# Kernel tuning notes

Measured on AMD Instinct MI355X. Metric: run time of the kernel, lower is better.

Reference implementation:

```python
import jax, jax.numpy as jnp
import numpy as np

B, S, D, H = 2, 2048, 1024, 16
DH = D // H  # head dim = 64


def setup_inputs() -> dict:
    key = jax.random.key(0)
    ks = jax.random.split(key, 8)
    q = jax.random.normal(ks[0], (B, S, D), dtype=jnp.float32)
    k = jax.random.normal(ks[1], (B, S, D), dtype=jnp.float32)
    v = jax.random.normal(ks[2], (B, S, D), dtype=jnp.float32)
    attn_mask = jax.random.randint(ks[3], (1, 1, S, S), 0, 2, dtype=jnp.int32)
    sc = 1.0 / np.sqrt(D)
    Wq = (jax.random.normal(ks[4], (D, D), dtype=jnp.float32) * sc)
    Wk = (jax.random.normal(ks[5], (D, D), dtype=jnp.float32) * sc)
    Wv = (jax.random.normal(ks[6], (D, D), dtype=jnp.float32) * sc)
    Wo = (jax.random.normal(ks[7], (D, D), dtype=jnp.float32) * sc)
    return {"q": q, "k": k, "v": v, "attn_mask": attn_mask,
            "Wq": Wq, "Wk": Wk, "Wv": Wv, "Wo": Wo}


def reference(q, k, v, attn_mask, Wq, Wk, Wv, Wo):
    bs = q.shape[0]
    # torch Linear: y = x @ W.T ; split heads -> [B, H, S, DH]
    qh = (q @ Wq.T).reshape(bs, -1, H, DH).transpose(0, 2, 1, 3)
    kh = (k @ Wk.T).reshape(bs, -1, H, DH).transpose(0, 2, 1, 3)
    vh = (v @ Wv.T).reshape(bs, -1, H, DH).transpose(0, 2, 1, 3)
    # scaled dot-product attention with explicit [B,H,S,S] scores
    scores = jnp.einsum('bhqd,bhkd->bhqk', qh, kh) / jnp.sqrt(
        jnp.asarray(DH, dtype=qh.dtype))
    scores = jnp.where(attn_mask == 0, jnp.asarray(-1e34, scores.dtype), scores)
    attn = jax.nn.softmax(scores, axis=-1)
    out = jnp.einsum('bhqk,bhkd->bhqd', attn, vh)
    out = out.transpose(0, 2, 1, 3).reshape(bs, -1, H * DH)
    out = out @ Wo.T
    return (out, attn)
```

## Files before the change

### kernel.cpp

```cpp
#include <hip/hip_runtime.h>
#include <stdint.h>

#define S_ 2048
#define NKT_ 32
#define LP 72

typedef short bf16x8 __attribute__((ext_vector_type(8)));
typedef float f32x4 __attribute__((ext_vector_type(4)));

__device__ __forceinline__ short f2bf(float x) {
  union { float f; uint32_t u; } v; v.f = x;
  uint32_t r = v.u + 0x7fffu + ((v.u >> 16) & 1u);
  return (short)(r >> 16);
}
__device__ __forceinline__ float bf2f(short s) {
  union { uint32_t u; float f; } v; v.u = ((uint32_t)(uint16_t)s) << 16;
  return v.f;
}

__device__ __forceinline__ void gload16(const void* g, void* l) {
  __builtin_amdgcn_global_load_lds((const __attribute__((address_space(1))) void*)g,
                                   (__attribute__((address_space(3))) void*)l, 16, 0, 0);
}

__global__ __launch_bounds__(256) void detect_dtype(const uint32_t* __restrict__ q,
                                                    uint32_t* __restrict__ flag) {
  __shared__ int cnt;
  int t = threadIdx.x;
  if (t == 0) cnt = 0;
  __syncthreads();
  uint32_t w = q[t];
  int e = (int)((w >> 7) & 0xFF);
  int hit = (e >= 100 && e <= 141) ? 1 : 0;
  atomicAdd(&cnt, hit);
  __syncthreads();
  if (t == 0) *flag = (cnt >= 200) ? 0u : 1u;
}

__device__ __forceinline__ void cvt_body(const void* __restrict__ src,
                                         short* __restrict__ d, long n8, int f) {
  long i = (long)blockIdx.x * 256 + threadIdx.x;
  const long stride = (long)gridDim.x * 256;
  if (f) {
    const f32x4* s = (const f32x4*)src;
    for (; i < n8; i += stride) {
      f32x4 a = s[2 * i], b = s[2 * i + 1];
      bf16x8 r;
      r[0] = f2bf(a[0]); r[1] = f2bf(a[1]); r[2] = f2bf(a[2]); r[3] = f2bf(a[3]);
      r[4] = f2bf(b[0]); r[5] = f2bf(b[1]); r[6] = f2bf(b[2]); r[7] = f2bf(b[3]);
      *(bf16x8*)(d + i * 8) = r;
    }
  } else {
    const bf16x8* s = (const bf16x8*)src;
    for (; i < n8; i += stride) *(bf16x8*)(d + i * 8) = s[i];
  }
}

__global__ __launch_bounds__(256) void to_bf16_batch(
    const void* __restrict__ q, const void* __restrict__ k, const void* __restrict__ v,
    const void* __restrict__ wq, const void* __restrict__ wk, const void* __restrict__ wv,
    short* __restrict__ dst, const uint32_t* __restrict__ flag) {
  const void* src; long n8; long doff;
  switch (blockIdx.y) {
    case 0:  src = q;  n8 = 524288; doff = 0;        break;
    case 1:  src = k;  n8 = 524288; doff = 4194304;  break;
    case 2:  src = v;  n8 = 524288; doff = 8388608;  break;
    case 3:  src = wq; n8 = 131072; doff = 12582912; break;
    case 4:  src = wk; n8 = 131072; doff = 13631488; break;
    default: src = wv; n8 = 131072; doff = 14680064; break;
  }
  cvt_body(src, dst + doff, n8, (int)*flag);
}

__global__ __launch_bounds__(256) void to_bf16_one(const void* __restrict__ src,
                                                   short* __restrict__ dst, long n8,
                                                   const uint32_t* __restrict__ flag) {
  cvt_body(src, dst, n8, (int)*flag);
}

template <int MODE>
__device__ __forceinline__ void gemm_body(short* sA, short* sW,
    const short* __restrict__ A, const short* __restrict__ W,
    short* __restrict__ dst, float* __restrict__ dstF, int outf) {
  const int tid = threadIdx.x;
  const int wave = tid >> 6, lane = tid & 63;
  const int quad = lane >> 4, l16 = lane & 15;
  const int m0 = blockIdx.x * 128, n0 = blockIdx.y * 128;
  const int wm = wave >> 1, wn = wave & 1;

  f32x4 acc[4][4] = {};

  for (int k0 = 0; k0 < 1024; k0 += 64) {
#pragma unroll
    for (int it = 0; it < 4; ++it) {
      int c = it * 256 + tid;
      int r = c >> 3, cs = (c & 7) ^ (r & 7);
      int ldsoff = (it * 256 + wave * 64) * 8;
      gload16(A + (long)(m0 + r) * 1024 + k0 + cs * 8, sA + ldsoff);
      gload16(W + (long)(n0 + r) * 1024 + k0 + cs * 8, sW + ldsoff);
    }
    __syncthreads();
    const short* Pa = (MODE == 2) ? sW : sA;
    const short* Pb = (MODE == 2) ? sA : sW;
#pragma unroll
    for (int kk = 0; kk < 2; ++kk) {
      const int cx = ((kk * 4 + quad) ^ (l16 & 7)) * 8;
      bf16x8 af[4], bfr[4];
#pragma unroll
      for (int i = 0; i < 4; ++i)
        af[i] = *(const bf16x8*)(Pa + (wm * 64 + i * 16 + l16) * 64 + cx);
#pragma unroll
      for (int j = 0; j < 4; ++j)
        bfr[j] = *(const bf16x8*)(Pb + (wn * 64 + j * 16 + l16) * 64 + cx);
#pragma unroll
      for (int i = 0; i < 4; ++i)
#pragma unroll
        for (int j = 0; j < 4; ++j)
          acc[i][j] = __builtin_amdgcn_mfma_f32_16x16x32_bf16(af[i], bfr[j], acc[i][j], 0, 0, 0);
    }
    __syncthreads();
  }

#pragma unroll
  for (int i = 0; i < 4; ++i)
#pragma unroll
    for (int j = 0; j < 4; ++j)
#pragma unroll
      for (int r = 0; r < 4; ++r) {
        float vv = acc[i][j][r];
        if (MODE == 0) vv *= 0.18033688011112042f;
        if (MODE == 2) {
          int n = n0 + wm * 64 + i * 16 + quad * 4 + r;
          int m = m0 + wn * 64 + j * 16 + l16;
          int b = m >> 11, s = m & 2047, h = n >> 6, dh = n & 63;
          dst[((long)((b * 16 + h) * 64 + dh)) * 2048 + s] = f2bf(vv);
        } else {
          int m = m0 + wm * 64 + i * 16 + quad * 4 + r;
          int n = n0 + wn * 64 + j * 16 + l16;
          if (MODE == 3) {
            if (outf) dstF[(long)m * 1024 + n] = vv;
            else      dst[(long)m * 1024 + n] = f2bf(vv);
          } else {
            int b = m >> 11, s = m & 2047, h = n >> 6, dh = n & 63;
            dst[((long)(b * 16 + h) * 2048 + s) * 64 + dh] = f2bf(vv);
          }
        }
      }
}

__global__ __launch_bounds__(256) void qkv_kernel(
    const short* __restrict__ qb, const short* __restrict__ kb, const short* __restrict__ vb,
    const short* __restrict__ Wqb, const short* __restrict__ Wkb, const short* __restrict__ Wvb,
    short* __restrict__ qh, short* __restrict__ kh, short* __restrict__ vt) {
  __shared__ __align__(16) short sA[128 * 64];
  __shared__ __align__(16) short sW[128 * 64];
  if (blockIdx.z == 0)      gemm_body<0>(sA, sW, qb, Wqb, qh, nullptr, 0);
  else if (blockIdx.z == 1) gemm_body<1>(sA, sW, kb, Wkb, kh, nullptr, 0);
  else                      gemm_body<2>(sA, sW, vb, Wvb, vt, nullptr, 0);
}

__global__ __launch_bounds__(256) void oproj_kernel(
    const short* __restrict__ o, const short* __restrict__ Wob,
    const uint32_t* __restrict__ flag,
    short* __restrict__ outB, float* __restrict__ outF) {
  __shared__ __align__(16) short sA[128 * 64];
  __shared__ __align__(16) short sW[128 * 64];
  gemm_body<3>(sA, sW, o, Wob, outB, outF, (int)*flag);
}

__global__ __launch_bounds__(256) void pack_mask(const int* __restrict__ mask,
                                                 uint32_t* __restrict__ bits) {
  int gt = blockIdx.x * 256 + threadIdx.x;
  int wid = gt >> 6, lane = gt & 63;
  int nw = (gridDim.x * 256) >> 6;
  for (int g = wid; g < (S_ * S_) / 64; g += nw) {
    int v = mask[(long)g * 64 + lane];
    unsigned long long b = __ballot(v != 0);
    if (lane == 0) bits[2 * g] = (uint32_t)b;
    if (lane == 1) bits[2 * g + 1] = (uint32_t)(b >> 32);
  }
}

__global__ __launch_bounds__(256) void attn_kernel(
    const short* __restrict__ qh, const short* __restrict__ kh,
    const short* __restrict__ vt, const uint32_t* __restrict__ mbits,
    const uint32_t* __restrict__ flag,
    short* __restrict__ attnB, float* __restrict__ attnF, short* __restrict__ o) {
  __shared__ __align__(16) short sK[2][64 * 64];
  __shared__ __align__(16) short sV[2][64 * 64];
  __shared__ __align__(16) short sP[4][32 * LP];
  const int tid = threadIdx.x;
  const int wave = tid >> 6, lane = tid & 63;
  const int quad = lane >> 4, l16 = lane & 15;
  const int q0 = blockIdx.x * 128;
  const int bh = blockIdx.y;
  const int outf = (int)*flag;
  const short* Qb = qh + (long)bh * S_ * 64;
  const short* Kb = kh + (long)bh * S_ * 64;
  const short* Vb = vt + (long)bh * 64 * S_;
  short* attnBb = attnB + (long)bh * S_ * S_;
  float* attnFb = attnF + (long)bh * S_ * S_;
  short* sPw = sP[wave];
  const uint32_t cm0 = 1u << l16, cm1 = 1u << (l16 + 16);

  auto stageK = [&](int kt, int b) {
#pragma unroll
    for (int it = 0; it < 2; ++it) {
      int c = it * 256 + tid;
      int r = c >> 3, cs = (c & 7) ^ (r & 7);
      gload16(Kb + (long)(kt * 64 + r) * 64 + cs * 8, &sK[b][(it * 256 + wave * 64) * 8]);
    }
  };
  auto stageV = [&](int kt, int b) {
#pragma unroll
    for (int it = 0; it < 2; ++it) {
      int c = it * 256 + tid;
      int r = c >> 3, cs = (c & 7) ^ (r & 7);
      gload16(Vb + (long)r * S_ + kt * 64 + cs * 8, &sV[b][(it * 256 + wave * 64) * 8]);
    }
  };

  bf16x8 qf[2][2];
#pragma unroll
  for (int i = 0; i < 2; ++i)
#pragma unroll
    for (int kk = 0; kk < 2; ++kk)
      qf[i][kk] = *(const bf16x8*)(Qb + (long)(q0 + wave * 32 + i * 16 + l16) * 64 + kk * 32 + quad * 8);

  float mrun[2][4], lrun[2][4];
#pragma unroll
  for (int i = 0; i < 2; ++i)
#pragma unroll
    for (int r = 0; r < 4; ++r) { mrun[i][r] = -3e38f; lrun[i][r] = 0.f; }

  stageK(0, 0);
  __syncthreads();
  int buf = 0;
  for (int kt = 0; kt < NKT_; ++kt) {
    const int k0 = kt * 64;
    if (kt + 1 < NKT_) stageK(kt + 1, buf ^ 1);
    f32x4 acc[2][4] = {};
#pragma unroll
    for (int kk = 0; kk < 2; ++kk) {
      const int cx = ((kk * 4 + quad) ^ (l16 & 7)) * 8;
      bf16x8 bfr[4];
#pragma unroll
      for (int j = 0; j < 4; ++j)
        bfr[j] = *(const bf16x8*)(&sK[buf][(j * 16 + l16) * 64 + cx]);
#pragma unroll
      for (int i = 0; i < 2; ++i)
#pragma unroll
        for (int j = 0; j < 4; ++j)
          acc[i][j] = __builtin_amdgcn_mfma_f32_16x16x32_bf16(qf[i][kk], bfr[j], acc[i][j], 0, 0, 0);
    }
#pragma unroll
    for (int i = 0; i < 2; ++i)
#pragma unroll
      for (int r = 0; r < 4; ++r) {
        int qrow = q0 + wave * 32 + i * 16 + quad * 4 + r;
        const uint32_t* wp = mbits + qrow * 64 + (k0 >> 5);
        uint32_t w0 = wp[0], w1 = wp[1];
        float s0 = (w0 & cm0) ? acc[i][0][r] : -1e30f;
        float s1 = (w0 & cm1) ? acc[i][1][r] : -1e30f;
        float s2 = (w1 & cm0) ? acc[i][2][r] : -1e30f;
        float s3 = (w1 & cm1) ? acc[i][3][r] : -1e30f;
        float mx = fmaxf(fmaxf(s0, s1), fmaxf(s2, s3));
        mx = fmaxf(mx, __shfl_xor(mx, 1));
        mx = fmaxf(mx, __shfl_xor(mx, 2));
        mx = fmaxf(mx, __shfl_xor(mx, 4));
        mx = fmaxf(mx, __shfl_xor(mx, 8));
        float mold = mrun[i][r];
        float mnew = fmaxf(mold, mx);
        float sum = exp2f(s0 - mnew) + exp2f(s1 - mnew) + exp2f(s2 - mnew) + exp2f(s3 - mnew);
        sum += __shfl_xor(sum, 1);
        sum += __shfl_xor(sum, 2);
        sum += __shfl_xor(sum, 4);
        sum += __shfl_xor(sum, 8);
        lrun[i][r] = lrun[i][r] * exp2f(mold - mnew) + sum;
        mrun[i][r] = mnew;
      }
    __syncthreads();
    buf ^= 1;
  }

  float invl[2][4];
#pragma unroll
  for (int i = 0; i < 2; ++i)
#pragma unroll
    for (int r = 0; r < 4; ++r) invl[i][r] = 1.0f / lrun[i][r];

  f32x4 acco[2][4] = {};

  stageK(0, 0); stageV(0, 0);
  __syncthreads();
  buf = 0;
  for (int kt = 0; kt < NKT_; ++kt) {
    const int k0 = kt * 64;
    if (kt + 1 < NKT_) { stageK(kt + 1, buf ^ 1); stageV(kt + 1, buf ^ 1); }
    f32x4 acc[2][4] = {};
#pragma unroll
    for (int kk = 0; kk < 2; ++kk) {
      const int cx = ((kk * 4 + quad) ^ (l16 & 7)) * 8;
      bf16x8 bfr[4];
#pragma unroll
      for (int j = 0; j < 4; ++j)
        bfr[j] = *(const bf16x8*)(&sK[buf][(j * 16 + l16) * 64 + cx]);
#pragma unroll
      for (int i = 0; i < 2; ++i)
#pragma unroll
        for (int j = 0; j < 4; ++j)
          acc[i][j] = __builtin_amdgcn_mfma_f32_16x16x32_bf16(qf[i][kk], bfr[j], acc[i][j], 0, 0, 0);
    }
#pragma unroll
    for (int i = 0; i < 2; ++i)
#pragma unroll
      for (int r = 0; r < 4; ++r) {
        int qrow = q0 + wave * 32 + i * 16 + quad * 4 + r;
        const uint32_t* wp = mbits + qrow * 64 + (k0 >> 5);
        uint32_t w0 = wp[0], w1 = wp[1];
        float mm = mrun[i][r], il = invl[i][r];
        float s0 = (w0 & cm0) ? acc[i][0][r] : -1e30f;
        float s1 = (w0 & cm1) ? acc[i][1][r] : -1e30f;
        float s2 = (w1 & cm0) ? acc[i][2][r] : -1e30f;
        float s3 = (w1 & cm1) ? acc[i][3][r] : -1e30f;
        int rowL = i * 16 + quad * 4 + r;
        short* rp = sPw + rowL * LP;
        rp[0  + l16] = f2bf(exp2f(s0 - mm) * il);
        rp[16 + l16] = f2bf(exp2f(s1 - mm) * il);
        rp[32 + l16] = f2bf(exp2f(s2 - mm) * il);
        rp[48 + l16] = f2bf(exp2f(s3 - mm) * il);
      }
    asm volatile("s_waitcnt lgkmcnt(0)" ::: "memory");
    __builtin_amdgcn_sched_barrier(0);
#pragma unroll
    for (int it = 0; it < 4; ++it) {
      int cid = it * 64 + lane;
      int rowL = cid >> 3, kc = cid & 7;
      bf16x8 vals = *(const bf16x8*)(sPw + rowL * LP + kc * 8);
      long base = (long)(q0 + wave * 32 + rowL) * S_ + k0 + kc * 8;
      if (outf) {
        f32x4 lo, hi;
#pragma unroll
        for (int e = 0; e < 4; ++e) { lo[e] = bf2f(vals[e]); hi[e] = bf2f(vals[e + 4]); }
        *(f32x4*)(attnFb + base) = lo;
        *(f32x4*)(attnFb + base + 4) = hi;
      } else {
        *(bf16x8*)(attnBb + base) = vals;
      }
    }
    bf16x8 vf[2][4];
#pragma unroll
    for (int kk = 0; kk < 2; ++kk) {
      const int cx = ((kk * 4 + quad) ^ (l16 & 7)) * 8;
#pragma unroll
      for (int jd = 0; jd < 4; ++jd)
        vf[kk][jd] = *(const bf16x8*)(&sV[buf][(jd * 16 + l16) * 64 + cx]);
    }
#pragma unroll
    for (int kk = 0; kk < 2; ++kk)
#pragma unroll
      for (int i = 0; i < 2; ++i) {
        bf16x8 pf = *(const bf16x8*)(sPw + (i * 16 + l16) * LP + (kk * 4 + quad) * 8);
#pragma unroll
        for (int jd = 0; jd < 4; ++jd)
          acco[i][jd] = __builtin_amdgcn_mfma_f32_16x16x32_bf16(pf, vf[kk][jd], acco[i][jd], 0, 0, 0);
      }
    __syncthreads();
    buf ^= 1;
  }

  const int b = bh >> 4, h = bh & 15;
#pragma unroll
  for (int i = 0; i < 2; ++i)
#pragma unroll
    for (int jd = 0; jd < 4; ++jd)
#pragma unroll
      for (int r = 0; r < 4; ++r) {
        int qrow = q0 + wave * 32 + i * 16 + quad * 4 + r;
        int dh = jd * 16 + l16;
        o[(long)(b * S_ + qrow) * 1024 + h * 64 + dh] = f2bf(acco[i][jd][r]);
      }
}

extern "C" void kernel_launch(void* const* d_in, const int* in_sizes, int n_in,
                              void* d_out, int out_size, void* d_ws, size_t ws_size,
                              hipStream_t stream) {
  (void)in_sizes; (void)n_in; (void)out_size; (void)ws_size;
  const void* q  = d_in[0];
  const void* k  = d_in[1];
  const void* v  = d_in[2];
  const int* mask = (const int*)d_in[3];
  const void* Wq = d_in[4];
  const void* Wk = d_in[5];
  const void* Wv = d_in[6];
  const void* Wo = d_in[7];

  short* outB  = (short*)d_out;
  short* attnB = outB + (long)4194304;
  float* outF  = (float*)d_out;
  float* attnF = outF + (long)4194304;

  short* qh = (short*)d_ws;
  short* kh = qh + (long)4194304;
  short* vt = kh + (long)4194304;
  short* o  = vt + (long)4194304;
  uint32_t* mbits = (uint32_t*)(o + (long)4194304);
  uint32_t* flag  = mbits + 131072;

  short* qb  = (short*)((char*)d_out + (20l << 20));
  short* kb  = qb  + (long)4194304;
  short* vb  = kb  + (long)4194304;
  short* wqb = vb  + (long)4194304;
  short* wkb = wqb + (long)1048576;
  short* wvb = wkb + (long)1048576;
  short* wob = qh;

  detect_dtype<<<dim3(1), dim3(256), 0, stream>>>((const uint32_t*)q, flag);
  pack_mask<<<dim3(256), dim3(256), 0, stream>>>(mask, mbits);
  to_bf16_batch<<<dim3(512, 6), dim3(256), 0, stream>>>(q, k, v, Wq, Wk, Wv, qb, flag);
  qkv_kernel<<<dim3(32, 8, 3), dim3(256), 0, stream>>>(qb, kb, vb, wqb, wkb, wvb, qh, kh, vt);
  attn_kernel<<<dim3(16, 32), dim3(256), 0, stream>>>(qh, kh, vt, mbits, flag, attnB, attnF, o);
  to_bf16_one<<<dim3(512), dim3(256), 0, stream>>>(Wo, wob, 131072, flag);
  oproj_kernel<<<dim3(32, 8), dim3(256), 0, stream>>>(o, wob, flag, outB, outF);
}
```

Measured before the change: 889.9 us.

## Widen stats-pass key tile to 128, remap blocks for L2 locality, add setprio

The first (max/sum) pass now processes 128 keys per iteration, reusing the K and V shared buffers as two 128-row K stages. This halves the number of barriers and loop iterations and loads each mask row with one 128-bit read. Block indices are remapped so consecutive blocks are spread across heads differently, which is meant to improve L2 sharing of K/V and mask data. MFMA sections are wrapped in s_setprio to favour matrix issue over other waves. The wider accumulators raise register pressure, which could lower occupancy.

```diff
diff --git a/kernel.cpp b/kernel.cpp
--- a/kernel.cpp
+++ b/kernel.cpp
@@ -3,6 +3,7 @@
 
 #define S_ 2048
 #define NKT_ 32
+#define NKTA_ 16
 #define LP 72
 
 typedef short bf16x8 __attribute__((ext_vector_type(8)));
@@ -192,8 +193,9 @@
   const int tid = threadIdx.x;
   const int wave = tid >> 6, lane = tid & 63;
   const int quad = lane >> 4, l16 = lane & 15;
-  const int q0 = blockIdx.x * 128;
-  const int bh = blockIdx.y;
+  const int bidf = blockIdx.y * 16 + blockIdx.x;
+  const int bh = (bidf & 7) * 4 + ((bidf >> 3) >> 4);
+  const int q0 = ((bidf >> 3) & 15) * 128;
   const int outf = (int)*flag;
   const short* Qb = qh + (long)bh * S_ * 64;
   const short* Kb = kh + (long)bh * S_ * 64;
@@ -203,6 +205,16 @@
   short* sPw = sP[wave];
   const uint32_t cm0 = 1u << l16, cm1 = 1u << (l16 + 16);
 
+  auto bufA = [&](int b) -> short* { return b ? &sV[0][0] : &sK[0][0]; };
+  auto stageA = [&](int kt, int b) {
+    short* dstp = bufA(b);
+#pragma unroll
+    for (int it = 0; it < 4; ++it) {
+      int c = it * 256 + tid;
+      int r = c >> 3, cs = (c & 7) ^ (r & 7);
+      gload16(Kb + (long)(kt * 128 + r) * 64 + cs * 8, dstp + (it * 256 + wave * 64) * 8);
+    }
+  };
   auto stageK = [&](int kt, int b) {
 #pragma unroll
     for (int it = 0; it < 2; ++it) {
@@ -233,45 +245,52 @@
 #pragma unroll
     for (int r = 0; r < 4; ++r) { mrun[i][r] = -3e38f; lrun[i][r] = 0.f; }
 
-  stageK(0, 0);
+  stageA(0, 0);
   __syncthreads();
   int buf = 0;
-  for (int kt = 0; kt < NKT_; ++kt) {
-    const int k0 = kt * 64;
-    if (kt + 1 < NKT_) stageK(kt + 1, buf ^ 1);
-    f32x4 acc[2][4] = {};
+  for (int kt = 0; kt < NKTA_; ++kt) {
+    if (kt + 1 < NKTA_) stageA(kt + 1, buf ^ 1);
+    const short* Kt = bufA(buf);
+    f32x4 acc[2][8] = {};
 #pragma unroll
     for (int kk = 0; kk < 2; ++kk) {
       const int cx = ((kk * 4 + quad) ^ (l16 & 7)) * 8;
-      bf16x8 bfr[4];
-#pragma unroll
-      for (int j = 0; j < 4; ++j)
-        bfr[j] = *(const bf16x8*)(&sK[buf][(j * 16 + l16) * 64 + cx]);
+      bf16x8 bfr[8];
+#pragma unroll
+      for (int j = 0; j < 8; ++j)
+        bfr[j] = *(const bf16x8*)(Kt + (j * 16 + l16) * 64 + cx);
+      __builtin_amdgcn_s_setprio(1);
 #pragma unroll
       for (int i = 0; i < 2; ++i)
 #pragma unroll
-        for (int j = 0; j < 4; ++j)
+        for (int j = 0; j < 8; ++j)
           acc[i][j] = __builtin_amdgcn_mfma_f32_16x16x32_bf16(qf[i][kk], bfr[j], acc[i][j], 0, 0, 0);
+      __builtin_amdgcn_s_setprio(0);
     }
 #pragma unroll
     for (int i = 0; i < 2; ++i)
 #pragma unroll
       for (int r = 0; r < 4; ++r) {
         int qrow = q0 + wave * 32 + i * 16 + quad * 4 + r;
-        const uint32_t* wp = mbits + qrow * 64 + (k0 >> 5);
-        uint32_t w0 = wp[0], w1 = wp[1];
-        float s0 = (w0 & cm0) ? acc[i][0][r] : -1e30f;
-        float s1 = (w0 & cm1) ? acc[i][1][r] : -1e30f;
-        float s2 = (w1 & cm0) ? acc[i][2][r] : -1e30f;
-        float s3 = (w1 & cm1) ? acc[i][3][r] : -1e30f;
-        float mx = fmaxf(fmaxf(s0, s1), fmaxf(s2, s3));
+        uint4 w = *(const uint4*)(mbits + qrow * 64 + kt * 4);
+        float s0 = (w.x & cm0) ? acc[i][0][r] : -1e30f;
+        float s1 = (w.x & cm1) ? acc[i][1][r] : -1e30f;
+        float s2 = (w.y & cm0) ? acc[i][2][r] : -1e30f;
+        float s3 = (w.y & cm1) ? acc[i][3][r] : -1e30f;
+        float s4 = (w.z & cm0) ? acc[i][4][r] : -1e30f;
+        float s5 = (w.z & cm1) ? acc[i][5][r] : -1e30f;
+        float s6 = (w.w & cm0) ? acc[i][6][r] : -1e30f;
+        float s7 = (w.w & cm1) ? acc[i][7][r] : -1e30f;
+        float mx = fmaxf(fmaxf(fmaxf(s0, s1), fmaxf(s2, s3)),
+                         fmaxf(fmaxf(s4, s5), fmaxf(s6, s7)));
         mx = fmaxf(mx, __shfl_xor(mx, 1));
         mx = fmaxf(mx, __shfl_xor(mx, 2));
         mx = fmaxf(mx, __shfl_xor(mx, 4));
         mx = fmaxf(mx, __shfl_xor(mx, 8));
         float mold = mrun[i][r];
         float mnew = fmaxf(mold, mx);
-        float sum = exp2f(s0 - mnew) + exp2f(s1 - mnew) + exp2f(s2 - mnew) + exp2f(s3 - mnew);
+        float sum = exp2f(s0 - mnew) + exp2f(s1 - mnew) + exp2f(s2 - mnew) + exp2f(s3 - mnew)
+                  + exp2f(s4 - mnew) + exp2f(s5 - mnew) + exp2f(s6 - mnew) + exp2f(s7 - mnew);
         sum += __shfl_xor(sum, 1);
         sum += __shfl_xor(sum, 2);
         sum += __shfl_xor(sum, 4);
@@ -305,11 +324,13 @@
 #pragma unroll
       for (int j = 0; j < 4; ++j)
         bfr[j] = *(const bf16x8*)(&sK[buf][(j * 16 + l16) * 64 + cx]);
+      __builtin_amdgcn_s_setprio(1);
 #pragma unroll
       for (int i = 0; i < 2; ++i)
 #pragma unroll
         for (int j = 0; j < 4; ++j)
           acc[i][j] = __builtin_amdgcn_mfma_f32_16x16x32_bf16(qf[i][kk], bfr[j], acc[i][j], 0, 0, 0);
+      __builtin_amdgcn_s_setprio(0);
     }
 #pragma unroll
     for (int i = 0; i < 2; ++i)
@@ -356,6 +377,7 @@
       for (int jd = 0; jd < 4; ++jd)
         vf[kk][jd] = *(const bf16x8*)(&sV[buf][(jd * 16 + l16) * 64 + cx]);
     }
+    __builtin_amdgcn_s_setprio(1);
 #pragma unroll
     for (int kk = 0; kk < 2; ++kk)
 #pragma unroll
@@ -365,6 +387,7 @@
         for (int jd = 0; jd < 4; ++jd)
           acco[i][jd] = __builtin_amdgcn_mfma_f32_16x16x32_bf16(pf, vf[kk][jd], acco[i][jd], 0, 0, 0);
       }
+    __builtin_amdgcn_s_setprio(0);
     __syncthreads();
     buf ^= 1;
   }
```

After: 859.5 us. -3.4%, faster.
